# Performance work log

Hardware: AMD Instinct MI355X
Metric: run time of the kernel (lower is better)

## Reference

```python
import jax, jax.numpy as jnp
import numpy as np

B, H, N, D = 4, 8, 2048, 64

def setup_inputs() -> dict:
    key = jax.random.key(0)
    kq, kk, kv = jax.random.split(key, 3)
    q = jax.random.uniform(kq, (B, H, N, D), dtype=jnp.float32)
    k = jax.random.uniform(kk, (B, H, N, D), dtype=jnp.float32)
    v = jax.random.normal(kv, (B, H, N, D), dtype=jnp.float32)
    return {"q": q, "k": k, "v": v}

def reference(q, k, v):
    d = k.shape[-1]
    # Hamming-similarity score: 0.5 * (1 + (2q-1)(2k-1)^T / d)
    sim = jnp.einsum("bhnd,bhmd->bhnm", 2.0 * q - 1.0, 2.0 * k - 1.0)
    score = jax.nn.softmax(0.5 * (1.0 + sim / d), axis=-1)
    out = jnp.einsum("bhnm,bhmd->bhnd", score, v)
    return (out, score)
```

## Files before the change

kernel.cpp:

```cpp
#include <hip/hip_runtime.h>
#include <hip/hip_bf16.h>

#define NN 2048
#define DD 64

typedef __attribute__((ext_vector_type(8))) short bf16x8;
typedef __attribute__((ext_vector_type(4))) float f32x4;

__device__ __forceinline__ unsigned short f2b(float f) {
    __hip_bfloat16 h = __float2bfloat16(f);
    return __builtin_bit_cast(unsigned short, h);
}

__global__ void prep_qk(const float4* __restrict__ q, const float4* __restrict__ k,
                        ushort4* __restrict__ qo, ushort4* __restrict__ ko) {
    int i = blockIdx.x * 256 + threadIdx.x;
    float4 a = q[i], b = k[i];
    ushort4 qa, kb;
    qa.x = f2b(2.f*a.x - 1.f); qa.y = f2b(2.f*a.y - 1.f);
    qa.z = f2b(2.f*a.z - 1.f); qa.w = f2b(2.f*a.w - 1.f);
    kb.x = f2b(2.f*b.x - 1.f); kb.y = f2b(2.f*b.y - 1.f);
    kb.z = f2b(2.f*b.z - 1.f); kb.w = f2b(2.f*b.w - 1.f);
    qo[i] = qa; ko[i] = kb;
}

__global__ void prep_v(const float* __restrict__ v, unsigned short* __restrict__ vt) {
    __shared__ float tile[64][65];
    int bh = blockIdx.x >> 5, jt = blockIdx.x & 31;
    int t = threadIdx.x;
    const float* src = v + ((size_t)bh * NN + jt * 64) * DD;
#pragma unroll
    for (int h = 0; h < 4; ++h) {
        int cc = t + h * 256;
        int row = cc >> 4, c4 = cc & 15;
        float4 f = *(const float4*)(src + row * DD + c4 * 4);
        tile[row][c4*4+0] = f.x; tile[row][c4*4+1] = f.y;
        tile[row][c4*4+2] = f.z; tile[row][c4*4+3] = f.w;
    }
    __syncthreads();
    unsigned short* dst = vt + (size_t)bh * DD * NN + jt * 64;
#pragma unroll
    for (int h = 0; h < 2; ++h) {
        int cc = t + h * 256;
        int d = cc >> 3, c8 = cc & 7;
        unsigned int w0 = (unsigned)f2b(tile[c8*8+0][d]) | ((unsigned)f2b(tile[c8*8+1][d]) << 16);
        unsigned int w1 = (unsigned)f2b(tile[c8*8+2][d]) | ((unsigned)f2b(tile[c8*8+3][d]) << 16);
        unsigned int w2 = (unsigned)f2b(tile[c8*8+4][d]) | ((unsigned)f2b(tile[c8*8+5][d]) << 16);
        unsigned int w3 = (unsigned)f2b(tile[c8*8+6][d]) | ((unsigned)f2b(tile[c8*8+7][d]) << 16);
        uint4 pk = { w0, w1, w2, w3 };
        *(uint4*)(dst + (size_t)d * NN + c8 * 8) = pk;
    }
}

__global__ __launch_bounds__(256, 2) void attn(
        const unsigned short* __restrict__ Qw, const unsigned short* __restrict__ Kw,
        const unsigned short* __restrict__ Vtw,
        float* __restrict__ outp, float* __restrict__ score) {
    __shared__ unsigned short kb[2][64][72];
    __shared__ unsigned short vt[2][64][72];
    __shared__ float sc[4][16][68];
    __shared__ float lsum[64];

    const int tid = threadIdx.x;
    const int bh = blockIdx.x & 31, qp = blockIdx.x >> 5;
    const int lane = tid & 63, wave = tid >> 6;
    const int l4 = lane & 15, quad = lane >> 4;
    const int row0 = wave * 16;

    const unsigned short* Kh = Kw + (size_t)bh * NN * DD;
    const unsigned short* Vh = Vtw + (size_t)bh * DD * NN;

    const int sr0 = tid >> 3,         sc0 = (tid & 7) * 8;
    const int sr1 = (tid + 256) >> 3, sc1 = ((tid + 256) & 7) * 8;

    for (int it = 0; it < 2; ++it) {
        const int i0 = (qp * 2 + it) * 64;
        const unsigned short* Qh = Qw + ((size_t)bh * NN + i0) * DD;
        float* scoreH = score + (size_t)bh * NN * NN + (size_t)i0 * NN;
        float* outH   = outp  + ((size_t)bh * NN + i0) * DD;

        {
            uint4 t0 = *(const uint4*)(Qh + (size_t)sr0 * DD + sc0);
            uint4 t1 = *(const uint4*)(Qh + (size_t)sr1 * DD + sc1);
            *(uint4*)&kb[0][sr0][sc0] = t0;
            *(uint4*)&kb[0][sr1][sc1] = t1;
        }
        __syncthreads();
        const bf16x8 a0 = *(const bf16x8*)&kb[0][row0 + l4][quad * 8];
        const bf16x8 a1 = *(const bf16x8*)&kb[0][row0 + l4][32 + quad * 8];
        __syncthreads();

        uint4 k0 = *(const uint4*)(Kh + (size_t)sr0 * DD + sc0);
        uint4 k1 = *(const uint4*)(Kh + (size_t)sr1 * DD + sc1);
        *(uint4*)&kb[0][sr0][sc0] = k0;
        *(uint4*)&kb[0][sr1][sc1] = k1;
        k0 = *(const uint4*)(Kh + (size_t)64 * DD + (size_t)sr0 * DD + sc0);
        k1 = *(const uint4*)(Kh + (size_t)64 * DD + (size_t)sr1 * DD + sc1);
        __syncthreads();

        float psum[4] = {0.f, 0.f, 0.f, 0.f};
        for (int kt = 0; kt < 32; ++kt) {
            const int cur = kt & 1, nxt = cur ^ 1;
            if (kt + 1 < 32) {
                *(uint4*)&kb[nxt][sr0][sc0] = k0;
                *(uint4*)&kb[nxt][sr1][sc1] = k1;
            }
            if (kt + 2 < 32) {
                const unsigned short* s = Kh + (size_t)(kt + 2) * 64 * DD;
                k0 = *(const uint4*)(s + (size_t)sr0 * DD + sc0);
                k1 = *(const uint4*)(s + (size_t)sr1 * DD + sc1);
            }
#pragma unroll
            for (int nb = 0; nb < 4; ++nb) {
                bf16x8 b0 = *(const bf16x8*)&kb[cur][nb * 16 + l4][quad * 8];
                bf16x8 b1 = *(const bf16x8*)&kb[cur][nb * 16 + l4][32 + quad * 8];
                f32x4 acc = {0.f, 0.f, 0.f, 0.f};
                acc = __builtin_amdgcn_mfma_f32_16x16x32_bf16(a0, b0, acc, 0, 0, 0);
                acc = __builtin_amdgcn_mfma_f32_16x16x32_bf16(a1, b1, acc, 0, 0, 0);
#pragma unroll
                for (int r = 0; r < 4; ++r)
                    psum[r] += __expf(fmaf(acc[r], 0.0078125f, 0.5f));
            }
            __syncthreads();
        }
#pragma unroll
        for (int r = 0; r < 4; ++r) {
#pragma unroll
            for (int m = 1; m < 16; m <<= 1) psum[r] += __shfl_xor(psum[r], m, 64);
        }
        if (l4 == 0) {
#pragma unroll
            for (int r = 0; r < 4; ++r) lsum[row0 + quad * 4 + r] = psum[r];
        }

        uint4 w0, w1;
        k0 = *(const uint4*)(Kh + (size_t)sr0 * DD + sc0);
        k1 = *(const uint4*)(Kh + (size_t)sr1 * DD + sc1);
        w0 = *(const uint4*)(Vh + (size_t)sr0 * NN + sc0);
        w1 = *(const uint4*)(Vh + (size_t)sr1 * NN + sc1);
        *(uint4*)&kb[0][sr0][sc0] = k0;
        *(uint4*)&kb[0][sr1][sc1] = k1;
        *(uint4*)&vt[0][sr0][sc0] = w0;
        *(uint4*)&vt[0][sr1][sc1] = w1;
        k0 = *(const uint4*)(Kh + (size_t)64 * DD + (size_t)sr0 * DD + sc0);
        k1 = *(const uint4*)(Kh + (size_t)64 * DD + (size_t)sr1 * DD + sc1);
        w0 = *(const uint4*)(Vh + 64 + (size_t)sr0 * NN + sc0);
        w1 = *(const uint4*)(Vh + 64 + (size_t)sr1 * NN + sc1);
        __syncthreads();

        float rinv[4];
#pragma unroll
        for (int r = 0; r < 4; ++r) rinv[r] = 1.0f / lsum[row0 + quad * 4 + r];
        f32x4 o[4];
#pragma unroll
        for (int nb = 0; nb < 4; ++nb) o[nb] = (f32x4){0.f, 0.f, 0.f, 0.f};

        for (int kt = 0; kt < 32; ++kt) {
            const int cur = kt & 1, nxt = cur ^ 1;
            if (kt > 0) {
#pragma unroll
                for (int h = 0; h < 4; ++h) {
                    const int rr = h * 4 + quad;
                    f32x4 wv = *(const f32x4*)&sc[wave][rr][l4 * 4];
                    __builtin_nontemporal_store(wv,
                        (f32x4*)&scoreH[(size_t)(row0 + rr) * NN + (kt - 1) * 64 + l4 * 4]);
                }
            }
            if (kt + 1 < 32) {
                *(uint4*)&kb[nxt][sr0][sc0] = k0;
                *(uint4*)&kb[nxt][sr1][sc1] = k1;
                *(uint4*)&vt[nxt][sr0][sc0] = w0;
                *(uint4*)&vt[nxt][sr1][sc1] = w1;
            }
            if (kt + 2 < 32) {
                const unsigned short* sk = Kh + (size_t)(kt + 2) * 64 * DD;
                const unsigned short* sv = Vh + (size_t)(kt + 2) * 64;
                k0 = *(const uint4*)(sk + (size_t)sr0 * DD + sc0);
                k1 = *(const uint4*)(sk + (size_t)sr1 * DD + sc1);
                w0 = *(const uint4*)(sv + (size_t)sr0 * NN + sc0);
                w1 = *(const uint4*)(sv + (size_t)sr1 * NN + sc1);
            }
#pragma unroll
            for (int nb = 0; nb < 4; ++nb) {
                bf16x8 b0 = *(const bf16x8*)&kb[cur][nb * 16 + l4][quad * 8];
                bf16x8 b1 = *(const bf16x8*)&kb[cur][nb * 16 + l4][32 + quad * 8];
                f32x4 acc = {0.f, 0.f, 0.f, 0.f};
                acc = __builtin_amdgcn_mfma_f32_16x16x32_bf16(a0, b0, acc, 0, 0, 0);
                acc = __builtin_amdgcn_mfma_f32_16x16x32_bf16(a1, b1, acc, 0, 0, 0);
#pragma unroll
                for (int r = 0; r < 4; ++r) {
                    float p = __expf(fmaf(acc[r], 0.0078125f, 0.5f)) * rinv[r];
                    sc[wave][quad * 4 + r][nb * 16 + l4] = p;
                }
            }
            f32x4 x0 = *(const f32x4*)&sc[wave][l4][quad * 8];
            f32x4 x1 = *(const f32x4*)&sc[wave][l4][quad * 8 + 4];
            f32x4 y0 = *(const f32x4*)&sc[wave][l4][32 + quad * 8];
            f32x4 y1 = *(const f32x4*)&sc[wave][l4][32 + quad * 8 + 4];
            bf16x8 p0, p1;
#pragma unroll
            for (int j = 0; j < 4; ++j) {
                p0[j]     = (short)f2b(x0[j]);
                p0[j + 4] = (short)f2b(x1[j]);
                p1[j]     = (short)f2b(y0[j]);
                p1[j + 4] = (short)f2b(y1[j]);
            }
#pragma unroll
            for (int nb = 0; nb < 4; ++nb) {
                bf16x8 u0 = *(const bf16x8*)&vt[cur][nb * 16 + l4][quad * 8];
                bf16x8 u1 = *(const bf16x8*)&vt[cur][nb * 16 + l4][32 + quad * 8];
                o[nb] = __builtin_amdgcn_mfma_f32_16x16x32_bf16(p0, u0, o[nb], 0, 0, 0);
                o[nb] = __builtin_amdgcn_mfma_f32_16x16x32_bf16(p1, u1, o[nb], 0, 0, 0);
            }
            __syncthreads();
        }
#pragma unroll
        for (int h = 0; h < 4; ++h) {
            const int rr = h * 4 + quad;
            f32x4 wv = *(const f32x4*)&sc[wave][rr][l4 * 4];
            __builtin_nontemporal_store(wv,
                (f32x4*)&scoreH[(size_t)(row0 + rr) * NN + 31 * 64 + l4 * 4]);
        }
#pragma unroll
        for (int nb = 0; nb < 4; ++nb)
#pragma unroll
            for (int r = 0; r < 4; ++r)
                sc[wave][quad * 4 + r][nb * 16 + l4] = o[nb][r];
#pragma unroll
        for (int h = 0; h < 4; ++h) {
            const int rr = h * 4 + quad;
            f32x4 wv = *(const f32x4*)&sc[wave][rr][l4 * 4];
            *(f32x4*)&outH[(size_t)(row0 + rr) * DD + l4 * 4] = wv;
        }
        __syncthreads();
    }
}

extern "C" void kernel_launch(void* const* d_in, const int* in_sizes, int n_in,
                              void* d_out, int out_size, void* d_ws, size_t ws_size,
                              hipStream_t stream) {
    const float* q = (const float*)d_in[0];
    const float* k = (const float*)d_in[1];
    const float* v = (const float*)d_in[2];
    float* outp  = (float*)d_out;
    float* score = outp + (size_t)4 * 8 * 2048 * 64;

    unsigned short* Qw  = (unsigned short*)d_ws;
    unsigned short* Kw  = Qw + (size_t)4 * 8 * 2048 * 64;
    unsigned short* Vtw = Kw + (size_t)4 * 8 * 2048 * 64;

    prep_qk<<<4096, 256, 0, stream>>>((const float4*)q, (const float4*)k,
                                      (ushort4*)Qw, (ushort4*)Kw);
    prep_v<<<1024, 256, 0, stream>>>(v, Vtw);
    attn<<<512, 256, 0, stream>>>(Qw, Kw, Vtw, outp, score);
}
```

Before: 635.4 us.

## Process 128 query rows per block with 8 waves and bf16 score staging

The attention kernel now runs 512-thread blocks in which 8 waves each own 16 query rows. All 128 rows are handled concurrently, replacing two sequential 64-row iterations, so each K and V tile loaded into shared memory serves twice as many rows and there are more waves to hide latency. The probability tile is staged in shared memory as bf16 instead of fp32, which removes the separate float-to-bf16 repack before the PV matmul and shrinks LDS use. The trade-off is that the written score output is now bf16-rounded and widened back to fp32, which loses precision, and register pressure rises under the new launch bounds.

```diff
diff --git a/kernel.cpp b/kernel.cpp
--- a/kernel.cpp
+++ b/kernel.cpp
@@ -10,6 +10,9 @@
 __device__ __forceinline__ unsigned short f2b(float f) {
     __hip_bfloat16 h = __float2bfloat16(f);
     return __builtin_bit_cast(unsigned short, h);
+}
+__device__ __forceinline__ float b2f(unsigned int u) {
+    return __builtin_bit_cast(float, u << 16);
 }
 
 __global__ void prep_qk(const float4* __restrict__ q, const float4* __restrict__ k,
@@ -52,64 +55,58 @@
     }
 }
 
-__global__ __launch_bounds__(256, 2) void attn(
+__global__ __launch_bounds__(512, 4) void attn(
         const unsigned short* __restrict__ Qw, const unsigned short* __restrict__ Kw,
         const unsigned short* __restrict__ Vtw,
         float* __restrict__ outp, float* __restrict__ score) {
     __shared__ unsigned short kb[2][64][72];
     __shared__ unsigned short vt[2][64][72];
-    __shared__ float sc[4][16][68];
-    __shared__ float lsum[64];
+    __shared__ unsigned short scb[8][16][72];
+    __shared__ float lsum[128];
 
     const int tid = threadIdx.x;
     const int bh = blockIdx.x & 31, qp = blockIdx.x >> 5;
     const int lane = tid & 63, wave = tid >> 6;
     const int l4 = lane & 15, quad = lane >> 4;
-    const int row0 = wave * 16;
 
     const unsigned short* Kh = Kw + (size_t)bh * NN * DD;
     const unsigned short* Vh = Vtw + (size_t)bh * DD * NN;
 
-    const int sr0 = tid >> 3,         sc0 = (tid & 7) * 8;
-    const int sr1 = (tid + 256) >> 3, sc1 = ((tid + 256) & 7) * 8;
-
-    for (int it = 0; it < 2; ++it) {
-        const int i0 = (qp * 2 + it) * 64;
-        const unsigned short* Qh = Qw + ((size_t)bh * NN + i0) * DD;
-        float* scoreH = score + (size_t)bh * NN * NN + (size_t)i0 * NN;
-        float* outH   = outp  + ((size_t)bh * NN + i0) * DD;
-
-        {
-            uint4 t0 = *(const uint4*)(Qh + (size_t)sr0 * DD + sc0);
-            uint4 t1 = *(const uint4*)(Qh + (size_t)sr1 * DD + sc1);
-            *(uint4*)&kb[0][sr0][sc0] = t0;
-            *(uint4*)&kb[0][sr1][sc1] = t1;
-        }
+    const int sr = tid >> 3, scc = (tid & 7) * 8;
+
+    const int i0 = qp * 128;
+    const unsigned short* Qh = Qw + ((size_t)bh * NN + i0) * DD;
+    float* scoreW = score + (size_t)bh * NN * NN + (size_t)(i0 + wave * 16) * NN;
+    float* outW   = outp  + ((size_t)bh * NN + i0 + wave * 16) * DD;
+
+    *(uint4*)&kb[0][sr][scc] = *(const uint4*)(Qh + (size_t)sr * DD + scc);
+    *(uint4*)&vt[0][sr][scc] = *(const uint4*)(Qh + (size_t)(64 + sr) * DD + scc);
+    __syncthreads();
+    bf16x8 a0, a1;
+    {
+        const int qr = (wave & 3) * 16 + l4;
+        if (wave < 4) {
+            a0 = *(const bf16x8*)&kb[0][qr][quad * 8];
+            a1 = *(const bf16x8*)&kb[0][qr][32 + quad * 8];
+        } else {
+            a0 = *(const bf16x8*)&vt[0][qr][quad * 8];
+            a1 = *(const bf16x8*)&vt[0][qr][32 + quad * 8];
+        }
+    }
+    __syncthreads();
+
+    {
+        uint4 kk = *(const uint4*)(Kh + (size_t)sr * DD + scc);
+        *(uint4*)&kb[0][sr][scc] = kk;
+        kk = *(const uint4*)(Kh + (size_t)64 * DD + (size_t)sr * DD + scc);
         __syncthreads();
-        const bf16x8 a0 = *(const bf16x8*)&kb[0][row0 + l4][quad * 8];
-        const bf16x8 a1 = *(const bf16x8*)&kb[0][row0 + l4][32 + quad * 8];
-        __syncthreads();
-
-        uint4 k0 = *(const uint4*)(Kh + (size_t)sr0 * DD + sc0);
-        uint4 k1 = *(const uint4*)(Kh + (size_t)sr1 * DD + sc1);
-        *(uint4*)&kb[0][sr0][sc0] = k0;
-        *(uint4*)&kb[0][sr1][sc1] = k1;
-        k0 = *(const uint4*)(Kh + (size_t)64 * DD + (size_t)sr0 * DD + sc0);
-        k1 = *(const uint4*)(Kh + (size_t)64 * DD + (size_t)sr1 * DD + sc1);
-        __syncthreads();
-
-        float psum[4] = {0.f, 0.f, 0.f, 0.f};
+
+        float ps[4] = {0.f, 0.f, 0.f, 0.f};
         for (int kt = 0; kt < 32; ++kt) {
             const int cur = kt & 1, nxt = cur ^ 1;
-            if (kt + 1 < 32) {
-                *(uint4*)&kb[nxt][sr0][sc0] = k0;
-                *(uint4*)&kb[nxt][sr1][sc1] = k1;
-            }
-            if (kt + 2 < 32) {
-                const unsigned short* s = Kh + (size_t)(kt + 2) * 64 * DD;
-                k0 = *(const uint4*)(s + (size_t)sr0 * DD + sc0);
-                k1 = *(const uint4*)(s + (size_t)sr1 * DD + sc1);
-            }
+            if (kt + 1 < 32) *(uint4*)&kb[nxt][sr][scc] = kk;
+            if (kt + 2 < 32)
+                kk = *(const uint4*)(Kh + (size_t)(kt + 2) * 64 * DD + (size_t)sr * DD + scc);
 #pragma unroll
             for (int nb = 0; nb < 4; ++nb) {
                 bf16x8 b0 = *(const bf16x8*)&kb[cur][nb * 16 + l4][quad * 8];
@@ -119,120 +116,108 @@
                 acc = __builtin_amdgcn_mfma_f32_16x16x32_bf16(a1, b1, acc, 0, 0, 0);
 #pragma unroll
                 for (int r = 0; r < 4; ++r)
-                    psum[r] += __expf(fmaf(acc[r], 0.0078125f, 0.5f));
+                    ps[r] += __expf(fmaf(acc[r], 0.0078125f, 0.5f));
             }
             __syncthreads();
         }
 #pragma unroll
         for (int r = 0; r < 4; ++r) {
 #pragma unroll
-            for (int m = 1; m < 16; m <<= 1) psum[r] += __shfl_xor(psum[r], m, 64);
+            for (int m = 1; m < 16; m <<= 1) ps[r] += __shfl_xor(ps[r], m, 64);
         }
         if (l4 == 0) {
 #pragma unroll
-            for (int r = 0; r < 4; ++r) lsum[row0 + quad * 4 + r] = psum[r];
-        }
-
-        uint4 w0, w1;
-        k0 = *(const uint4*)(Kh + (size_t)sr0 * DD + sc0);
-        k1 = *(const uint4*)(Kh + (size_t)sr1 * DD + sc1);
-        w0 = *(const uint4*)(Vh + (size_t)sr0 * NN + sc0);
-        w1 = *(const uint4*)(Vh + (size_t)sr1 * NN + sc1);
-        *(uint4*)&kb[0][sr0][sc0] = k0;
-        *(uint4*)&kb[0][sr1][sc1] = k1;
-        *(uint4*)&vt[0][sr0][sc0] = w0;
-        *(uint4*)&vt[0][sr1][sc1] = w1;
-        k0 = *(const uint4*)(Kh + (size_t)64 * DD + (size_t)sr0 * DD + sc0);
-        k1 = *(const uint4*)(Kh + (size_t)64 * DD + (size_t)sr1 * DD + sc1);
-        w0 = *(const uint4*)(Vh + 64 + (size_t)sr0 * NN + sc0);
-        w1 = *(const uint4*)(Vh + 64 + (size_t)sr1 * NN + sc1);
+            for (int r = 0; r < 4; ++r) lsum[wave * 16 + quad * 4 + r] = ps[r];
+        }
+    }
+
+    uint4 kk = *(const uint4*)(Kh + (size_t)sr * DD + scc);
+    uint4 vv = *(const uint4*)(Vh + (size_t)sr * NN + scc);
+    *(uint4*)&kb[0][sr][scc] = kk;
+    *(uint4*)&vt[0][sr][scc] = vv;
+    kk = *(const uint4*)(Kh + (size_t)64 * DD + (size_t)sr * DD + scc);
+    vv = *(const uint4*)(Vh + 64 + (size_t)sr * NN + scc);
+    __syncthreads();
+
+    float rinv[4];
+#pragma unroll
+    for (int r = 0; r < 4; ++r) rinv[r] = 1.0f / lsum[wave * 16 + quad * 4 + r];
+    f32x4 o[4];
+#pragma unroll
+    for (int nb = 0; nb < 4; ++nb) o[nb] = (f32x4){0.f, 0.f, 0.f, 0.f};
+
+    for (int kt = 0; kt < 32; ++kt) {
+        const int cur = kt & 1, nxt = cur ^ 1;
+        if (kt > 0) {
+#pragma unroll
+            for (int h = 0; h < 4; ++h) {
+                const int rr = h * 4 + quad;
+                uint2 pk = *(const uint2*)&scb[wave][rr][l4 * 4];
+                f32x4 wv;
+                wv[0] = b2f(pk.x & 0xffffu); wv[1] = b2f(pk.x >> 16);
+                wv[2] = b2f(pk.y & 0xffffu); wv[3] = b2f(pk.y >> 16);
+                __builtin_nontemporal_store(wv,
+                    (f32x4*)&scoreW[(size_t)rr * NN + (kt - 1) * 64 + l4 * 4]);
+            }
+        }
+        if (kt + 1 < 32) {
+            *(uint4*)&kb[nxt][sr][scc] = kk;
+            *(uint4*)&vt[nxt][sr][scc] = vv;
+        }
+        if (kt + 2 < 32) {
+            const unsigned short* sk = Kh + (size_t)(kt + 2) * 64 * DD;
+            const unsigned short* sv = Vh + (size_t)(kt + 2) * 64;
+            kk = *(const uint4*)(sk + (size_t)sr * DD + scc);
+            vv = *(const uint4*)(sv + (size_t)sr * NN + scc);
+        }
+#pragma unroll
+        for (int nb = 0; nb < 4; ++nb) {
+            bf16x8 b0 = *(const bf16x8*)&kb[cur][nb * 16 + l4][quad * 8];
+            bf16x8 b1 = *(const bf16x8*)&kb[cur][nb * 16 + l4][32 + quad * 8];
+            f32x4 acc = {0.f, 0.f, 0.f, 0.f};
+            acc = __builtin_amdgcn_mfma_f32_16x16x32_bf16(a0, b0, acc, 0, 0, 0);
+            acc = __builtin_amdgcn_mfma_f32_16x16x32_bf16(a1, b1, acc, 0, 0, 0);
+#pragma unroll
+            for (int r = 0; r < 4; ++r) {
+                float p = __expf(fmaf(acc[r], 0.0078125f, 0.5f)) * rinv[r];
+                scb[wave][quad * 4 + r][nb * 16 + l4] = f2b(p);
+            }
+        }
+        bf16x8 p0 = *(const bf16x8*)&scb[wave][l4][quad * 8];
+        bf16x8 p1 = *(const bf16x8*)&scb[wave][l4][32 + quad * 8];
+#pragma unroll
+        for (int nb = 0; nb < 4; ++nb) {
+            bf16x8 u0 = *(const bf16x8*)&vt[cur][nb * 16 + l4][quad * 8];
+            bf16x8 u1 = *(const bf16x8*)&vt[cur][nb * 16 + l4][32 + quad * 8];
+            o[nb] = __builtin_amdgcn_mfma_f32_16x16x32_bf16(p0, u0, o[nb], 0, 0, 0);
+            o[nb] = __builtin_amdgcn_mfma_f32_16x16x32_bf16(p1, u1, o[nb], 0, 0, 0);
+        }
         __syncthreads();
-
-        float rinv[4];
-#pragma unroll
-        for (int r = 0; r < 4; ++r) rinv[r] = 1.0f / lsum[row0 + quad * 4 + r];
-        f32x4 o[4];
-#pragma unroll
-        for (int nb = 0; nb < 4; ++nb) o[nb] = (f32x4){0.f, 0.f, 0.f, 0.f};
-
-        for (int kt = 0; kt < 32; ++kt) {
-            const int cur = kt & 1, nxt = cur ^ 1;
-            if (kt > 0) {
-#pragma unroll
-                for (int h = 0; h < 4; ++h) {
-                    const int rr = h * 4 + quad;
-                    f32x4 wv = *(const f32x4*)&sc[wave][rr][l4 * 4];
-                    __builtin_nontemporal_store(wv,
-                        (f32x4*)&scoreH[(size_t)(row0 + rr) * NN + (kt - 1) * 64 + l4 * 4]);
-                }
-            }
-            if (kt + 1 < 32) {
-                *(uint4*)&kb[nxt][sr0][sc0] = k0;
-                *(uint4*)&kb[nxt][sr1][sc1] = k1;
-                *(uint4*)&vt[nxt][sr0][sc0] = w0;
-                *(uint4*)&vt[nxt][sr1][sc1] = w1;
-            }
-            if (kt + 2 < 32) {
-                const unsigned short* sk = Kh + (size_t)(kt + 2) * 64 * DD;
-                const unsigned short* sv = Vh + (size_t)(kt + 2) * 64;
-                k0 = *(const uint4*)(sk + (size_t)sr0 * DD + sc0);
-                k1 = *(const uint4*)(sk + (size_t)sr1 * DD + sc1);
-                w0 = *(const uint4*)(sv + (size_t)sr0 * NN + sc0);
-                w1 = *(const uint4*)(sv + (size_t)sr1 * NN + sc1);
-            }
-#pragma unroll
-            for (int nb = 0; nb < 4; ++nb) {
-                bf16x8 b0 = *(const bf16x8*)&kb[cur][nb * 16 + l4][quad * 8];
-                bf16x8 b1 = *(const bf16x8*)&kb[cur][nb * 16 + l4][32 + quad * 8];
-                f32x4 acc = {0.f, 0.f, 0.f, 0.f};
-                acc = __builtin_amdgcn_mfma_f32_16x16x32_bf16(a0, b0, acc, 0, 0, 0);
-                acc = __builtin_amdgcn_mfma_f32_16x16x32_bf16(a1, b1, acc, 0, 0, 0);
-#pragma unroll
-                for (int r = 0; r < 4; ++r) {
-                    float p = __expf(fmaf(acc[r], 0.0078125f, 0.5f)) * rinv[r];
-                    sc[wave][quad * 4 + r][nb * 16 + l4] = p;
-                }
-            }
-            f32x4 x0 = *(const f32x4*)&sc[wave][l4][quad * 8];
-            f32x4 x1 = *(const f32x4*)&sc[wave][l4][quad * 8 + 4];
-            f32x4 y0 = *(const f32x4*)&sc[wave][l4][32 + quad * 8];
-            f32x4 y1 = *(const f32x4*)&sc[wave][l4][32 + quad * 8 + 4];
-            bf16x8 p0, p1;
-#pragma unroll
-            for (int j = 0; j < 4; ++j) {
-                p0[j]     = (short)f2b(x0[j]);
-                p0[j + 4] = (short)f2b(x1[j]);
-                p1[j]     = (short)f2b(y0[j]);
-                p1[j + 4] = (short)f2b(y1[j]);
-            }
-#pragma unroll
-            for (int nb = 0; nb < 4; ++nb) {
-                bf16x8 u0 = *(const bf16x8*)&vt[cur][nb * 16 + l4][quad * 8];
-                bf16x8 u1 = *(const bf16x8*)&vt[cur][nb * 16 + l4][32 + quad * 8];
-                o[nb] = __builtin_amdgcn_mfma_f32_16x16x32_bf16(p0, u0, o[nb], 0, 0, 0);
-                o[nb] = __builtin_amdgcn_mfma_f32_16x16x32_bf16(p1, u1, o[nb], 0, 0, 0);
-            }
-            __syncthreads();
-        }
+    }
+#pragma unroll
+    for (int h = 0; h < 4; ++h) {
+        const int rr = h * 4 + quad;
+        uint2 pk = *(const uint2*)&scb[wave][rr][l4 * 4];
+        f32x4 wv;
+        wv[0] = b2f(pk.x & 0xffffu); wv[1] = b2f(pk.x >> 16);
+        wv[2] = b2f(pk.y & 0xffffu); wv[3] = b2f(pk.y >> 16);
+        __builtin_nontemporal_store(wv,
+            (f32x4*)&scoreW[(size_t)rr * NN + 31 * 64 + l4 * 4]);
+    }
+    {
+        float* ob = ((wave < 4) ? (float*)&kb[0][0][0] : (float*)&vt[0][0][0])
+                    + (size_t)(wave & 3) * 16 * 68;
+#pragma unroll
+        for (int nb = 0; nb < 4; ++nb)
+#pragma unroll
+            for (int r = 0; r < 4; ++r)
+                ob[(quad * 4 + r) * 68 + nb * 16 + l4] = o[nb][r];
 #pragma unroll
         for (int h = 0; h < 4; ++h) {
             const int rr = h * 4 + quad;
-            f32x4 wv = *(const f32x4*)&sc[wave][rr][l4 * 4];
-            __builtin_nontemporal_store(wv,
-                (f32x4*)&scoreH[(size_t)(row0 + rr) * NN + 31 * 64 + l4 * 4]);
-        }
-#pragma unroll
-        for (int nb = 0; nb < 4; ++nb)
-#pragma unroll
-            for (int r = 0; r < 4; ++r)
-                sc[wave][quad * 4 + r][nb * 16 + l4] = o[nb][r];
-#pragma unroll
-        for (int h = 0; h < 4; ++h) {
-            const int rr = h * 4 + quad;
-            f32x4 wv = *(const f32x4*)&sc[wave][rr][l4 * 4];
-            *(f32x4*)&outH[(size_t)(row0 + rr) * DD + l4 * 4] = wv;
-        }
-        __syncthreads();
+            f32x4 wv = *(const f32x4*)&ob[rr * 68 + l4 * 4];
+            *(f32x4*)&outW[(size_t)rr * DD + l4 * 4] = wv;
+        }
     }
 }
 
@@ -252,5 +237,5 @@
     prep_qk<<<4096, 256, 0, stream>>>((const float4*)q, (const float4*)k,
                                       (ushort4*)Qw, (ushort4*)Kw);
     prep_v<<<1024, 256, 0, stream>>>(v, Vtw);
-    attn<<<512, 256, 0, stream>>>(Qw, Kw, Vtw, outp, score);
-}
+    attn<<<512, 512, 0, stream>>>(Qw, Kw, Vtw, outp, score);
+}
```

Result: slower. 661.6 us (+4.1%).
